# Kernel tuning notes

Hardware: AMD Instinct MI355X
Metric: run time of the kernel (lower is better)

## Reference

```python
import math
import jax, jax.numpy as jnp
import numpy as np


def setup_inputs() -> dict:
    key = jax.random.key(0)
    kq, kk, kv = jax.random.split(key, 3)
    bs, n_tok, n_heads, width = 2, 2048, 8, 64
    deg = 32  # neighbors per dst token -> coo_cnt_max
    q = jax.random.normal(kq, (bs, n_tok, n_heads, width), dtype=jnp.float32)
    k = jax.random.normal(kk, (bs, n_tok, n_heads, width), dtype=jnp.float32)
    v = jax.random.normal(kv, (bs, n_tok, n_heads, width), dtype=jnp.float32)
    rng = np.random.default_rng(0)
    dst = np.repeat(np.arange(n_tok), deg)            # [cl]
    src = rng.integers(0, n_tok, size=n_tok * deg)    # [cl]
    sm = np.tile(np.arange(deg), n_tok)               # [cl], unique per dst
    coo = jnp.asarray(np.stack([dst, src, sm], axis=1), dtype=jnp.int32)  # [cl,3]
    return {"q": q, "k": k, "v": v, "coo": coo, "coo_cnt_max": deg}


def reference(q, k, v, coo, coo_cnt_max):
    bs, n_tok, n_heads, width = q.shape
    dst, src, sm = coo[:, 0], coo[:, 1], coo[:, 2]
    # [b, h, t, w] layout
    qq = q.transpose(0, 2, 1, 3)
    kk = k.transpose(0, 2, 1, 3)
    vv = v.transpose(0, 2, 1, 3)
    scale = -1.0 / math.sqrt(width)
    # per-edge negative scaled L1 distance: [b, h, cl]
    ww = jnp.sum(jnp.abs(qq[:, :, dst, :] - kk[:, :, src, :]), axis=-1) * scale
    neg_big = jnp.asarray(-1e32, dtype=q.dtype)
    # scatter edge scores into dense padded attention slots: [b, h, t, cnt+1]
    attn = jnp.full((bs, n_heads, n_tok, coo_cnt_max + 1), neg_big, dtype=q.dtype)
    attn = attn.at[:, :, dst, sm].set(ww)
    attn_sm = jax.nn.softmax(attn, axis=-1)
    # scatter values into padded neighbor-value tensor: [b, h, t, cnt+1, w]
    vw = jnp.zeros((bs, n_heads, n_tok, coo_cnt_max + 1, width), dtype=q.dtype)
    vw = vw.at[:, :, dst, sm, :].set(vv[:, :, src, :])
    vo = jnp.einsum('bhds,bhdsw->bdhw', attn_sm, vw)
    # only dst tokens appearing in coo receive output; others stay zero
    vout = jnp.zeros_like(v).at[:, dst, :, :].set(vo[:, dst, :, :])
    return vout
```

## Files before the change

kernel.cpp:

```cpp
#include <hip/hip_runtime.h>
#include <hip/hip_bf16.h>

#define BS   2
#define NT   2048
#define NH   8
#define WD   64
#define DEG  32

#define PK_ROWS   (BS * 4 * NT)
#define PK_ROW_B  512
#define PK_UINTS  (PK_ROWS * (PK_ROW_B / 4))

typedef _Float16 half2_t __attribute__((ext_vector_type(2)));

#if defined(__has_builtin)
#if __has_builtin(__builtin_amdgcn_fdot2)
#define HAVE_FDOT2 1
#endif
#endif

__device__ __forceinline__ unsigned short f2h(float f) {
    _Float16 h = (_Float16)f;
    unsigned short u; __builtin_memcpy(&u, &h, 2); return u;
}
__device__ __forceinline__ half2_t u2h2(unsigned int w) {
    half2_t r; __builtin_memcpy(&r, &w, 4); return r;
}
__device__ __forceinline__ unsigned int h22u(half2_t h) {
    unsigned int u; __builtin_memcpy(&u, &h, 4); return u;
}
__device__ __forceinline__ half2_t habs2(half2_t x) {
    unsigned int u = h22u(x) & 0x7fff7fffu;
    return u2h2(u);
}

__global__ __launch_bounds__(256) void pack_kv_f16(
    const float* __restrict__ k,
    const float* __restrict__ v,
    unsigned int* __restrict__ packed)
{
    const int u    = blockIdx.x * 256 + threadIdx.x;
    const int row  = u >> 7;
    const int pos  = u & 127;
    const int part = pos >> 6;
    const int e    = pos & 63;
    const int s    = row & (NT - 1);
    const int hp   = (row >> 11) & 3;
    const int b    = row >> 13;
    const int elem = e * 2;
    const int h_in = elem >> 6;
    const int w0   = elem & 63;

    const float* src = (part == 0 ? k : v)
        + (((size_t)(b * NT + s) * NH + hp * 2 + h_in) << 6) + w0;
    float2 f = *(const float2*)src;
    packed[u] = (unsigned int)f2h(f.x) | ((unsigned int)f2h(f.y) << 16);
}

__global__ __launch_bounds__(64) void l1attn_main_f16(
    const float* __restrict__ q,
    const unsigned int* __restrict__ packed,
    const int* __restrict__ coo,
    float* __restrict__ out)
{
    const int bid   = blockIdx.x;
    const int combo = bid & 7;
    const int hp    = combo & 3;
    const int b     = combo >> 2;
    const int t     = bid >> 3;
    const int ln    = threadIdx.x;
    const int hw    = ln >> 5;
    const int l     = ln & 31;

    __shared__ int          s_src[DEG];
    __shared__ unsigned int s_q[64];
    __shared__ unsigned int s_k[DEG * 64];

    if (ln < DEG) {
        s_src[ln] = coo[(t * DEG + ln) * 3 + 1];
    }
    {
        const float2* qrow = (const float2*)
            (q + ((size_t)(b * NT + t) * NH + hp * 2) * WD);
        float2 qv = qrow[ln];
        s_q[ln] = (unsigned int)f2h(qv.x) | ((unsigned int)f2h(qv.y) << 16);
    }
    __syncthreads();

    const size_t combo_base = (size_t)((b * 4 + hp) * NT) * (PK_ROW_B / 4);

    {
        const int rsub = ln >> 4;
        const int c    = ln & 15;
        #pragma unroll
        for (int r = 0; r < 8; ++r) {
            const int j = 4 * r + rsub;
            const int s = s_src[j];
            const int chunk = (c + j) & 15;
            const char* gaddr = (const char*)(packed + combo_base)
                              + (size_t)s * PK_ROW_B + chunk * 16;
            char* laddr = (char*)s_k + 4 * r * 256;
            __builtin_amdgcn_global_load_lds(
                (const __attribute__((address_space(1))) void*)gaddr,
                (__attribute__((address_space(3))) void*)laddr,
                16, 0, 0);
        }
    }

    const int jr = l >> 3;
    const int m8 = l & 7;
    uint4 vr[8];
    {
        const char* vbase = (const char*)(packed + combo_base)
                          + (16 + hw * 8) * 16 + m8 * 16;
        #pragma unroll
        for (int i = 0; i < 8; ++i) {
            const int sv = s_src[4 * i + jr];
            vr[i] = *(const uint4*)(vbase + (size_t)sv * PK_ROW_B);
        }
    }

    asm volatile("s_waitcnt vmcnt(8)" ::: "memory");

    float acc = 0.f;
#ifdef HAVE_FDOT2
    const half2_t one2 = {(_Float16)1.0f, (_Float16)1.0f};
#endif
    #pragma unroll
    for (int i = 0; i < 8; ++i) {
        const int slot = ((hw * 8 + i) - l) & 15;
        uint4 c = *(const uint4*)((const char*)s_k + l * 256 + slot * 16);
        const unsigned int ws[4] = {c.x, c.y, c.z, c.w};
        #pragma unroll
        for (int mm = 0; mm < 4; ++mm) {
            half2_t kh = u2h2(ws[mm]);
            half2_t qh = u2h2(s_q[hw * 32 + i * 4 + mm]);
            half2_t ad = habs2(qh - kh);
#ifdef HAVE_FDOT2
            acc = __builtin_amdgcn_fdot2(ad, one2, acc, false);
#else
            acc += (float)ad.x + (float)ad.y;
#endif
        }
    }
    float logit = -0.125f * acc;

    float mx = logit;
    #pragma unroll
    for (int d = 16; d >= 1; d >>= 1) mx = fmaxf(mx, __shfl_xor(mx, d));
    float e = __expf(logit - mx);
    float ssum = e;
    #pragma unroll
    for (int d = 16; d >= 1; d >>= 1) ssum += __shfl_xor(ssum, d);
    const float p = e / ssum;

    int p2i;
    {
        _Float16 ph = (_Float16)p;
        half2_t p2 = {ph, ph};
        p2i = h22u(p2);
    }
    half2_t b0 = {(_Float16)0.0f, (_Float16)0.0f};
    half2_t b1 = b0, b2 = b0, b3 = b0;
    #pragma unroll
    for (int i = 0; i < 8; ++i) {
        const int pj2i = __shfl(p2i, 4 * i + jr, 32);
        half2_t pj2 = u2h2(pj2i);
        b0 = __builtin_elementwise_fma(pj2, u2h2(vr[i].x), b0);
        b1 = __builtin_elementwise_fma(pj2, u2h2(vr[i].y), b1);
        b2 = __builtin_elementwise_fma(pj2, u2h2(vr[i].z), b2);
        b3 = __builtin_elementwise_fma(pj2, u2h2(vr[i].w), b3);
    }
    #pragma unroll
    for (int d = 8; d <= 16; d <<= 1) {
        unsigned int u0 = h22u(b0), u1 = h22u(b1);
        unsigned int u2 = h22u(b2), u3 = h22u(b3);
        b0 = b0 + u2h2((unsigned int)__shfl_xor((int)u0, d));
        b1 = b1 + u2h2((unsigned int)__shfl_xor((int)u1, d));
        b2 = b2 + u2h2((unsigned int)__shfl_xor((int)u2, d));
        b3 = b3 + u2h2((unsigned int)__shfl_xor((int)u3, d));
    }

    if (jr == 0) {
        const int h = hp * 2 + hw;
        float* ob = out + ((size_t)(b * NT + t) * NH + h) * WD + 8 * m8;
        *(float4*)(ob)     = make_float4((float)b0.x, (float)b0.y,
                                         (float)b1.x, (float)b1.y);
        *(float4*)(ob + 4) = make_float4((float)b2.x, (float)b2.y,
                                         (float)b3.x, (float)b3.y);
    }
}

__global__ __launch_bounds__(64) void l1attn_sparse_fp32(
    const float* __restrict__ q,
    const float* __restrict__ k,
    const float* __restrict__ v,
    const int* __restrict__ coo,
    float* __restrict__ out)
{
    const int bid   = blockIdx.x;
    const int combo = bid & 7;
    const int hp    = combo & 3;
    const int b     = combo >> 2;
    const int t     = bid >> 3;
    const int ln    = threadIdx.x;
    const int hw    = ln >> 5;
    const int l     = ln & 31;

    __shared__ int   s_src[DEG];
    __shared__ float s_q[2 * WD];
    __shared__ float s_k[DEG * 2 * WD];

    if (ln < DEG) s_src[ln] = coo[(t * DEG + ln) * 3 + 1];
    {
        const float2* qrow = (const float2*)
            (q + ((size_t)(b * NT + t) * NH + hp * 2) * WD);
        float2 qv = qrow[ln];
        s_q[2 * ln] = qv.x; s_q[2 * ln + 1] = qv.y;
    }
    __syncthreads();
    {
        #pragma unroll
        for (int r = 0; r < 16; ++r) {
            const int j = 2 * r + hw;
            const int s = s_src[j];
            const int chunk = (l + j) & 31;
            const float* gaddr = k + ((size_t)(b * NT + s) * NH + hp * 2) * WD
                               + chunk * 4;
            float* laddr = s_k + 2 * r * (2 * WD);
            __builtin_amdgcn_global_load_lds(
                (const __attribute__((address_space(1))) void*)gaddr,
                (__attribute__((address_space(3))) void*)laddr, 16, 0, 0);
        }
    }
    const int h  = hp * 2 + hw;
    const int jg = l >> 4;
    const int wq = l & 15;
    float4 vr[16];
    #pragma unroll
    for (int i = 0; i < 16; ++i) {
        const int sv = s_src[2 * i + jg];
        vr[i] = *(const float4*)(v + ((size_t)(b * NT + sv) * NH + h) * WD + 4 * wq);
    }
    __syncthreads();
    const float* qh = s_q + hw * WD;
    float acc = 0.f;
    #pragma unroll
    for (int i = 0; i < 16; ++i) {
        const int slot = ((hw * 16 + i) - l) & 31;
        float4 kv = *(const float4*)(s_k + l * (2 * WD) + slot * 4);
        const int wb = i * 4;
        acc += fabsf(qh[wb] - kv.x) + fabsf(qh[wb + 1] - kv.y)
             + fabsf(qh[wb + 2] - kv.z) + fabsf(qh[wb + 3] - kv.w);
    }
    float logit = -0.125f * acc;
    float m = logit;
    #pragma unroll
    for (int d = 16; d >= 1; d >>= 1) m = fmaxf(m, __shfl_xor(m, d));
    float e = __expf(logit - m);
    float ssum = e;
    #pragma unroll
    for (int d = 16; d >= 1; d >>= 1) ssum += __shfl_xor(ssum, d);
    const float p = e / ssum;
    float4 o4 = make_float4(0.f, 0.f, 0.f, 0.f);
    #pragma unroll
    for (int i = 0; i < 16; ++i) {
        const float pj = __shfl(p, 2 * i + jg, 32);
        o4.x += pj * vr[i].x; o4.y += pj * vr[i].y;
        o4.z += pj * vr[i].z; o4.w += pj * vr[i].w;
    }
    o4.x += __shfl_xor(o4.x, 16); o4.y += __shfl_xor(o4.y, 16);
    o4.z += __shfl_xor(o4.z, 16); o4.w += __shfl_xor(o4.w, 16);
    if (jg == 0)
        *(float4*)(out + ((size_t)(b * NT + t) * NH + h) * WD + 4 * wq) = o4;
}

extern "C" void kernel_launch(void* const* d_in, const int* in_sizes, int n_in,
                              void* d_out, int out_size, void* d_ws, size_t ws_size,
                              hipStream_t stream) {
    const float* q   = (const float*)d_in[0];
    const float* k   = (const float*)d_in[1];
    const float* v   = (const float*)d_in[2];
    const int*   coo = (const int*)d_in[3];
    float*       o   = (float*)d_out;

    if (ws_size >= (size_t)PK_UINTS * 4) {
        unsigned int* packed = (unsigned int*)d_ws;
        hipLaunchKernelGGL(pack_kv_f16, dim3(PK_UINTS / 256), dim3(256), 0,
                           stream, k, v, packed);
        hipLaunchKernelGGL(l1attn_main_f16, dim3(BS * NT * 4), dim3(64), 0,
                           stream, q, packed, coo, o);
    } else {
        hipLaunchKernelGGL(l1attn_sparse_fp32, dim3(BS * NT * 4), dim3(64), 0,
                           stream, q, k, v, coo, o);
    }
}
```

Before: 96.64 us.

## Quantize V to int8 with per-row scale to halve value gather traffic

The pack kernel now stores V as biased uint8 with a per-row (token, head-pair) absmax scale table, replacing fp16. The main kernel gathers half as many V bytes per neighbor, decodes the bytes with the 0x6400 fp16 magic trick, and accumulates in fp32. The scale is folded into the softmax weight and the bias is removed by subtracting 1152*sum(p). This cuts the memory traffic of the random value gathers and the pack-kernel writes, at the cost of int8 precision loss on V and an extra scale lookup per edge.

```diff
diff --git a/kernel.cpp b/kernel.cpp
--- a/kernel.cpp
+++ b/kernel.cpp
@@ -10,6 +10,7 @@
 #define PK_ROWS   (BS * 4 * NT)
 #define PK_ROW_B  512
 #define PK_UINTS  (PK_ROWS * (PK_ROW_B / 4))
+#define SV_BYTES  (PK_ROWS * 4)
 
 typedef _Float16 half2_t __attribute__((ext_vector_type(2)));
 
@@ -34,32 +35,45 @@
     return u2h2(u);
 }
 
-__global__ __launch_bounds__(256) void pack_kv_f16(
+__global__ __launch_bounds__(256) void pack_kv_i8v(
     const float* __restrict__ k,
     const float* __restrict__ v,
-    unsigned int* __restrict__ packed)
+    unsigned int* __restrict__ packed,
+    float* __restrict__ svtab)
 {
-    const int u    = blockIdx.x * 256 + threadIdx.x;
-    const int row  = u >> 7;
-    const int pos  = u & 127;
-    const int part = pos >> 6;
-    const int e    = pos & 63;
-    const int s    = row & (NT - 1);
-    const int hp   = (row >> 11) & 3;
-    const int b    = row >> 13;
-    const int elem = e * 2;
-    const int h_in = elem >> 6;
-    const int w0   = elem & 63;
-
-    const float* src = (part == 0 ? k : v)
-        + (((size_t)(b * NT + s) * NH + hp * 2 + h_in) << 6) + w0;
-    float2 f = *(const float2*)src;
-    packed[u] = (unsigned int)f2h(f.x) | ((unsigned int)f2h(f.y) << 16);
-}
-
-__global__ __launch_bounds__(64) void l1attn_main_f16(
+    const int wid = (blockIdx.x * 256 + threadIdx.x) >> 6;
+    const int ln  = threadIdx.x & 63;
+    const int s   = wid & (NT - 1);
+    const int hp  = (wid >> 11) & 3;
+    const int b   = wid >> 13;
+    const int h_in = ln >> 5;
+    const int w0   = (2 * ln) & 63;
+
+    const size_t src_off =
+        (((size_t)(b * NT + s) * NH + hp * 2 + h_in) << 6) + w0;
+    const float2 kf = *(const float2*)(k + src_off);
+    const float2 vf = *(const float2*)(v + src_off);
+
+    packed[(size_t)wid * 128 + ln] =
+        (unsigned int)f2h(kf.x) | ((unsigned int)f2h(kf.y) << 16);
+
+    float m = fmaxf(fabsf(vf.x), fabsf(vf.y));
+    #pragma unroll
+    for (int d = 32; d >= 1; d >>= 1) m = fmaxf(m, __shfl_xor(m, d));
+    const float inv = (m > 0.f) ? 127.0f / m : 0.f;
+    const int i0 = (int)rintf(vf.x * inv) + 128;
+    const int i1 = (int)rintf(vf.y * inv) + 128;
+    unsigned short* vdst = (unsigned short*)
+        ((char*)packed + (size_t)wid * PK_ROW_B + 256);
+    vdst[ln] = (unsigned short)(i0 | (i1 << 8));
+
+    if (ln == 0) svtab[wid] = m * (1.0f / 127.0f);
+}
+
+__global__ __launch_bounds__(64) void l1attn_main_i8v(
     const float* __restrict__ q,
     const unsigned int* __restrict__ packed,
+    const float* __restrict__ svtab,
     const int* __restrict__ coo,
     float* __restrict__ out)
 {
@@ -89,6 +103,9 @@
 
     const size_t combo_base = (size_t)((b * 4 + hp) * NT) * (PK_ROW_B / 4);
 
+    const float sv_l = svtab[(b * 4 + hp) * NT + s_src[l]];
+    asm volatile("" ::: "memory");
+
     {
         const int rsub = ln >> 4;
         const int c    = ln & 15;
@@ -106,21 +123,22 @@
                 16, 0, 0);
         }
     }
-
-    const int jr = l >> 3;
-    const int m8 = l & 7;
-    uint4 vr[8];
+    asm volatile("" ::: "memory");
+
+    const int rg = l >> 2;
+    const int m4 = l & 3;
+    uint4 vr[4];
     {
         const char* vbase = (const char*)(packed + combo_base)
-                          + (16 + hw * 8) * 16 + m8 * 16;
-        #pragma unroll
-        for (int i = 0; i < 8; ++i) {
-            const int sv = s_src[4 * i + jr];
+                          + 256 + hw * 64 + m4 * 16;
+        #pragma unroll
+        for (int i = 0; i < 4; ++i) {
+            const int sv = s_src[8 * i + rg];
             vr[i] = *(const uint4*)(vbase + (size_t)sv * PK_ROW_B);
         }
     }
 
-    asm volatile("s_waitcnt vmcnt(8)" ::: "memory");
+    asm volatile("s_waitcnt vmcnt(4)" ::: "memory");
 
     float acc = 0.f;
 #ifdef HAVE_FDOT2
@@ -152,42 +170,56 @@
     float ssum = e;
     #pragma unroll
     for (int d = 16; d >= 1; d >>= 1) ssum += __shfl_xor(ssum, d);
-    const float p = e / ssum;
-
-    int p2i;
-    {
-        _Float16 ph = (_Float16)p;
-        half2_t p2 = {ph, ph};
-        p2i = h22u(p2);
-    }
-    half2_t b0 = {(_Float16)0.0f, (_Float16)0.0f};
-    half2_t b1 = b0, b2 = b0, b3 = b0;
-    #pragma unroll
-    for (int i = 0; i < 8; ++i) {
-        const int pj2i = __shfl(p2i, 4 * i + jr, 32);
-        half2_t pj2 = u2h2(pj2i);
-        b0 = __builtin_elementwise_fma(pj2, u2h2(vr[i].x), b0);
-        b1 = __builtin_elementwise_fma(pj2, u2h2(vr[i].y), b1);
-        b2 = __builtin_elementwise_fma(pj2, u2h2(vr[i].z), b2);
-        b3 = __builtin_elementwise_fma(pj2, u2h2(vr[i].w), b3);
-    }
-    #pragma unroll
-    for (int d = 8; d <= 16; d <<= 1) {
-        unsigned int u0 = h22u(b0), u1 = h22u(b1);
-        unsigned int u2 = h22u(b2), u3 = h22u(b3);
-        b0 = b0 + u2h2((unsigned int)__shfl_xor((int)u0, d));
-        b1 = b1 + u2h2((unsigned int)__shfl_xor((int)u1, d));
-        b2 = b2 + u2h2((unsigned int)__shfl_xor((int)u2, d));
-        b3 = b3 + u2h2((unsigned int)__shfl_xor((int)u3, d));
-    }
-
-    if (jr == 0) {
+    const float p  = e / ssum;
+    const float pp = p * sv_l;
+
+    float oev[4][2], ood[4][2];
+    #pragma unroll
+    for (int w = 0; w < 4; ++w) {
+        oev[w][0] = 0.f; oev[w][1] = 0.f; ood[w][0] = 0.f; ood[w][1] = 0.f;
+    }
+    float S = 0.f;
+    #pragma unroll
+    for (int i = 0; i < 4; ++i) {
+        const float pj = __shfl(pp, 8 * i + rg, 32);
+        S += pj;
+        const unsigned int ws[4] = {vr[i].x, vr[i].y, vr[i].z, vr[i].w};
+        #pragma unroll
+        for (int w = 0; w < 4; ++w) {
+            const unsigned int wv = ws[w];
+            half2_t he = u2h2((wv & 0x00ff00ffu) | 0x64006400u);
+            half2_t ho = u2h2(((wv >> 8) & 0x00ff00ffu) | 0x64006400u);
+            oev[w][0] = fmaf(pj, (float)he.x, oev[w][0]);
+            oev[w][1] = fmaf(pj, (float)he.y, oev[w][1]);
+            ood[w][0] = fmaf(pj, (float)ho.x, ood[w][0]);
+            ood[w][1] = fmaf(pj, (float)ho.y, ood[w][1]);
+        }
+    }
+    const float corr = 1152.0f * S;
+    #pragma unroll
+    for (int w = 0; w < 4; ++w) {
+        oev[w][0] -= corr; oev[w][1] -= corr;
+        ood[w][0] -= corr; ood[w][1] -= corr;
+    }
+    #pragma unroll
+    for (int d = 4; d <= 16; d <<= 1) {
+        #pragma unroll
+        for (int w = 0; w < 4; ++w) {
+            oev[w][0] += __shfl_xor(oev[w][0], d);
+            oev[w][1] += __shfl_xor(oev[w][1], d);
+            ood[w][0] += __shfl_xor(ood[w][0], d);
+            ood[w][1] += __shfl_xor(ood[w][1], d);
+        }
+    }
+
+    if (rg == 0) {
         const int h = hp * 2 + hw;
-        float* ob = out + ((size_t)(b * NT + t) * NH + h) * WD + 8 * m8;
-        *(float4*)(ob)     = make_float4((float)b0.x, (float)b0.y,
-                                         (float)b1.x, (float)b1.y);
-        *(float4*)(ob + 4) = make_float4((float)b2.x, (float)b2.y,
-                                         (float)b3.x, (float)b3.y);
+        float* ob = out + ((size_t)(b * NT + t) * NH + h) * WD + 16 * m4;
+        #pragma unroll
+        for (int w = 0; w < 4; ++w) {
+            *(float4*)(ob + 4 * w) = make_float4(
+                oev[w][0], ood[w][0], oev[w][1], ood[w][1]);
+        }
     }
 }
 
@@ -284,12 +316,13 @@
     const int*   coo = (const int*)d_in[3];
     float*       o   = (float*)d_out;
 
-    if (ws_size >= (size_t)PK_UINTS * 4) {
+    if (ws_size >= (size_t)PK_UINTS * 4 + SV_BYTES) {
         unsigned int* packed = (unsigned int*)d_ws;
-        hipLaunchKernelGGL(pack_kv_f16, dim3(PK_UINTS / 256), dim3(256), 0,
-                           stream, k, v, packed);
-        hipLaunchKernelGGL(l1attn_main_f16, dim3(BS * NT * 4), dim3(64), 0,
-                           stream, q, packed, coo, o);
+        float* svtab = (float*)((char*)d_ws + (size_t)PK_UINTS * 4);
+        hipLaunchKernelGGL(pack_kv_i8v, dim3(PK_ROWS / 4), dim3(256), 0,
+                           stream, k, v, packed, svtab);
+        hipLaunchKernelGGL(l1attn_main_i8v, dim3(BS * NT * 4), dim3(64), 0,
+                           stream, q, packed, svtab, coo, o);
     } else {
         hipLaunchKernelGGL(l1attn_sparse_fp32, dim3(BS * NT * 4), dim3(64), 0,
                            stream, q, k, v, coo, o);
```

After: 100.9 us. +4.4%, slower.
